# Performance work log

Hardware: AMD Instinct MI355X
Metric: run time of the kernel (lower is better)

## Reference

```python
import jax, jax.numpy as jnp
import numpy as np

N = 10000; E = 320000
DIM = 176; ATT = 16; SH_HEADS = 16; TH = 4; NH = SH_HEADS + TH; VD = DIM // SH_HEADS
LMAX = 3; NSPH = (LMAX + 1) ** 2; ZDIM = 16; RDIM = 16
RSTART = 0.8; CUT = 5.0; NLAYERS = 2


def _ln(x):
    mu = jnp.mean(x, axis=-1, keepdims=True)
    dx = x - mu
    var = jnp.mean(dx ** 2, axis=-1, keepdims=True)
    return dx * (1e-6 + var) ** (-0.5)


def _sph(v):
    # real spherical harmonics up to l=3, unnormalized overall scale, [E,16]
    x, y, z = v[..., 0], v[..., 1], v[..., 2]
    s3 = np.float32(np.sqrt(3.0)); s15 = np.float32(np.sqrt(15.0))
    c1 = np.float32(np.sqrt(5.0 / 8.0)); c2 = np.float32(np.sqrt(3.0 / 8.0))
    x2, y2, z2 = x * x, y * y, z * z
    return jnp.stack([
        jnp.ones_like(x),
        x, y, z,
        s3 * x * y, s3 * y * z, 0.5 * (3.0 * z2 - 1.0), s3 * x * z, 0.5 * s3 * (x2 - y2),
        c1 * y * (3.0 * x2 - y2), s15 * x * y * z, c2 * y * (5.0 * z2 - 1.0),
        0.5 * z * (5.0 * z2 - 3.0), c2 * x * (5.0 * z2 - 1.0),
        0.5 * s15 * z * (x2 - y2), c1 * x * (x2 - 3.0 * y2),
    ], axis=-1)


def setup_inputs() -> dict:
    key = jax.random.key(0)
    ks = jax.random.split(key, 32)

    def rn(k, shape):
        fan_in = shape[0] if len(shape) > 1 else shape[0]
        return jax.random.normal(k, shape, dtype=jnp.float32) / np.float32(np.sqrt(shape[0]))

    species = jax.random.randint(ks[0], (N,), 0, 64)
    edge_src = jax.random.randint(ks[1], (E,), 0, N)
    edge_dst = jax.random.randint(ks[2], (E,), 0, N)
    distances = RSTART + (CUT - RSTART) * jax.random.uniform(ks[3], (E,), dtype=jnp.float32)
    raw = jax.random.normal(ks[4], (E, 3), dtype=jnp.float32)
    dirn = raw / jnp.linalg.norm(raw, axis=-1, keepdims=True)
    vec = dirn * distances[:, None]
    switch = 0.5 * (jnp.cos(jnp.pi * distances / CUT) + 1.0)

    inp = {
        'species': species, 'distances': distances, 'switch': switch,
        'edge_src': edge_src, 'edge_dst': edge_dst, 'vec': vec,
        'z_table': jax.random.normal(ks[5], (64, ZDIM), dtype=jnp.float32),
        'w_species': rn(ks[6], (ZDIM, DIM)),
        'pos_w1_0': rn(ks[7], (RDIM, 2 * ATT)), 'pos_b1_0': jnp.zeros((2 * ATT,), jnp.float32),
        'pos_w2_0': rn(ks[8], (2 * ATT, ATT)), 'pos_b2_0': jnp.zeros((ATT,), jnp.float32),
        'wq_0': rn(ks[9], (DIM, NH * ATT)), 'wk_0': rn(ks[10], (DIM, NH * ATT)),
        'wv_0': rn(ks[11], (DIM, SH_HEADS * VD)),
        'upd_w_0': rn(ks[12], (2 * DIM, DIM)), 'upd_b_0': jnp.zeros((DIM,), jnp.float32),
        'pos_w1_1': rn(ks[13], (RDIM + TH * (LMAX + 1), 2 * ATT)), 'pos_b1_1': jnp.zeros((2 * ATT,), jnp.float32),
        'pos_w2_1': rn(ks[14], (2 * ATT, ATT)), 'pos_b2_1': jnp.zeros((ATT,), jnp.float32),
        'wq_1': rn(ks[15], (DIM, NH * ATT)), 'wk_1': rn(ks[16], (DIM, NH * ATT)),
        'wv_1': rn(ks[17], (DIM, SH_HEADS * VD)),
        'upd_w_1': rn(ks[18], (2 * DIM, DIM)), 'upd_b_1': jnp.zeros((DIM,), jnp.float32),
    }
    return inp


def reference(species, distances, switch, edge_src, edge_dst, vec,
              z_table, w_species,
              pos_w1_0, pos_b1_0, pos_w2_0, pos_b2_0, wq_0, wk_0, wv_0, upd_w_0, upd_b_0,
              pos_w1_1, pos_b1_1, pos_w2_1, pos_b2_1, wq_1, wk_1, wv_1, upd_w_1, upd_b_1):
    Nn = species.shape[0]
    Zi = z_table[species]                      # [N, ZDIM] species encoding
    xi = _ln(Zi @ w_species)                   # [N, DIM]

    vhat = vec / distances[:, None]
    Yij = _sph(vhat)                           # [E, NSPH]
    ls = np.repeat(np.arange(LMAX + 1), 2 * np.arange(LMAX + 1) + 1)
    parity = jnp.asarray(((-1.0) ** ls).astype(np.float32))  # [NSPH]

    centers = jnp.linspace(RSTART, CUT, RDIM, dtype=jnp.float32)
    sigma = np.float32((CUT - RSTART) / (RDIM - 1))
    radial = jnp.exp(-(((distances[:, None] - centers) / sigma) ** 2))  # [E, RDIM]

    Vi = jnp.zeros((Nn, TH, NSPH), jnp.float32)
    pos = [(pos_w1_0, pos_b1_0, pos_w2_0, pos_b2_0), (pos_w1_1, pos_b1_1, pos_w2_1, pos_b2_1)]
    att = [(wq_0, wk_0, wv_0, upd_w_0, upd_b_0), (wq_1, wk_1, wv_1, upd_w_1, upd_b_1)]
    inv_sqrt_d = np.float32(1.0 / np.sqrt(ATT))

    for layer in range(NLAYERS):
        pw1, pb1, pw2, pb2 = pos[layer]
        wq, wk, wv, uw, ub = att[layer]
        if layer == 0:
            ur = radial
        else:
            # tensor relative positional features: [E, TH, NSPH]
            xij2 = (Vi[edge_dst] + (parity * Vi)[edge_src]) * Yij[:, None, :]
            us = [xij2[:, :, l * l:(l + 1) * (l + 1)].sum(axis=-1) for l in range(LMAX + 1)]
            ur = jnp.concatenate([radial] + us, axis=-1)
        w = jax.nn.swish(ur @ pw1 + pb1) @ pw2 + pb2     # [E, ATT] positional encoding
        q = (xi @ wq).reshape(Nn, NH, ATT)
        k = (xi @ wk).reshape(Nn, NH, ATT)
        # multiplicative relative positional attention coefficients [E, NH]
        aij = jnp.einsum('ehd,ed->eh', q[edge_dst] * k[edge_src], w) * (switch[:, None] * inv_sqrt_d)
        a_s, a_t = aij[:, :SH_HEADS], aij[:, SH_HEADS:]
        v = (xi @ wv).reshape(Nn, SH_HEADS, VD)
        mi = jax.ops.segment_sum(a_s[:, :, None] * v[edge_src], edge_dst, num_segments=Nn)  # [N,SH,VD]
        Vi = Vi + jax.ops.segment_sum(
            a_t[:, :, None] * (Yij[:, None, :] + parity * Vi[edge_src]), edge_dst, num_segments=Nn)
        ui = jnp.concatenate([xi, mi.reshape(Nn, -1)], axis=-1)
        xi = _ln(xi + ui @ uw + ub)
    return xi
```

## Files before the change

kernel.cpp:

```cpp
#include <hip/hip_runtime.h>
#include <hip/hip_bf16.h>
#include <math.h>

#define N_NODES 10000
#define N_PAD   10048
#define N_EDGES 320000
#define DIM     176
#define ATT     16
#define SH_HEADS 16
#define THH     4
#define NH      20
#define VD      11
#define ZDIM    16
#define RDIM    16
#define QK_W    (NH*ATT)
#define QKV_W   816
#define UI_W    (2*DIM)
#define KQ      192
#define SIGINV  3.5714285714285716f
#define RSTEP   0.28f

typedef unsigned short ushort_t;
typedef __attribute__((ext_vector_type(8))) short bf16x8;
typedef __attribute__((ext_vector_type(4))) float f32x4;


__device__ __forceinline__ ushort_t f2bf(float f) {
    __hip_bfloat16 b = __float2bfloat16(f);
    return *(ushort_t*)&b;
}

__device__ __forceinline__ float bf2f(ushort_t u) {
    return __uint_as_float(((unsigned)u) << 16);
}

__device__ __forceinline__ void sph16(float x, float y, float z, float* Y) {
    const float s3  = 1.7320508075688772f;
    const float s15 = 3.872983346207417f;
    const float c1  = 0.7905694150420949f;
    const float c2  = 0.6123724356957945f;
    float x2 = x*x, y2 = y*y, z2 = z*z;
    Y[0]  = 1.0f;
    Y[1]  = x;
    Y[2]  = y;
    Y[3]  = z;
    Y[4]  = s3 * x * y;
    Y[5]  = s3 * y * z;
    Y[6]  = 0.5f * (3.0f * z2 - 1.0f);
    Y[7]  = s3 * x * z;
    Y[8]  = 0.5f * s3 * (x2 - y2);
    Y[9]  = c1 * y * (3.0f * x2 - y2);
    Y[10] = s15 * x * y * z;
    Y[11] = c2 * y * (5.0f * z2 - 1.0f);
    Y[12] = 0.5f * z * (5.0f * z2 - 3.0f);
    Y[13] = c2 * x * (5.0f * z2 - 1.0f);
    Y[14] = 0.5f * s15 * z * (x2 - y2);
    Y[15] = c1 * x * (x2 - 3.0f * y2);
}

__device__ __forceinline__ void unpack8(const uint4 u, float* f) {
    f[0] = __uint_as_float(u.x << 16);
    f[1] = __uint_as_float(u.x & 0xffff0000u);
    f[2] = __uint_as_float(u.y << 16);
    f[3] = __uint_as_float(u.y & 0xffff0000u);
    f[4] = __uint_as_float(u.z << 16);
    f[5] = __uint_as_float(u.z & 0xffff0000u);
    f[6] = __uint_as_float(u.w << 16);
    f[7] = __uint_as_float(u.w & 0xffff0000u);
}


__global__ __launch_bounds__(256) void k_deg(const int* edst, int* deg) {
    int e = blockIdx.x * 256 + threadIdx.x;
    if (e < N_EDGES) atomicAdd(&deg[edst[e]], 1);
}

__global__ __launch_bounds__(1024) void k_scan1(const int* deg, int* incl, int* bsum) {
    __shared__ int sd[1024];
    int b = blockIdx.x, tid = threadIdx.x;
    int gi = b * 1024 + tid;
    int v = (gi < N_NODES) ? deg[gi] : 0;
    sd[tid] = v;
    __syncthreads();
    for (int s = 1; s < 1024; s <<= 1) {
        int add = (tid >= s) ? sd[tid - s] : 0;
        __syncthreads();
        sd[tid] += add;
        __syncthreads();
    }
    if (gi < N_NODES) incl[gi] = sd[tid];
    if (tid == 1023) bsum[b] = sd[1023];
}

__global__ __launch_bounds__(1024) void k_scan3(const int* deg, const int* incl, const int* bsum,
                                                int* off, int* cursor) {
    __shared__ int bpre_s;
    int b = blockIdx.x, tid = threadIdx.x;
    if (tid == 0) {
        int acc = 0;
        for (int k = 0; k < b; k++) acc += bsum[k];
        bpre_s = acc;
    }
    __syncthreads();
    int gi = b * 1024 + tid;
    if (gi < N_NODES) {
        int e = bpre_s + incl[gi];
        off[gi + 1] = e;
        cursor[gi]  = e - deg[gi];
    }
    if (gi == 0) off[0] = 0;
}

__global__ __launch_bounds__(256) void k_scatter(const int* edst, int* cursor, int* elist) {
    int e = blockIdx.x * 256 + threadIdx.x;
    if (e < N_EDGES) {
        int p = atomicAdd(&cursor[edst[e]], 1);
        elist[p] = e;
    }
}

__global__ __launch_bounds__(256) void k_reorder(const int* elist, const int* esrc, const int* edst,
        const float* dist, const float* swit, const float* vec,
        int* src_c, int* dst_c, float* dist_c, float* sc_c, float* Yf) {
    int i = blockIdx.x * 256 + threadIdx.x;
    if (i >= N_EDGES) return;
    int e = elist[i];
    float d = dist[e];
    float inv = 1.0f / d;
    float vx = vec[(size_t)e*3 + 0] * inv;
    float vy = vec[(size_t)e*3 + 1] * inv;
    float vz = vec[(size_t)e*3 + 2] * inv;
    src_c[i]  = esrc[e];
    dst_c[i]  = edst[e];
    dist_c[i] = d;
    sc_c[i]   = swit[e] * 0.25f;
    float Y[16];
    sph16(vx, vy, vz, Y);
    #pragma unroll
    for (int m = 0; m < 16; m += 4)
        *(float4*)&Yf[(size_t)i * 16 + m] = make_float4(Y[m], Y[m+1], Y[m+2], Y[m+3]);
}


__device__ __forceinline__ void prep_qkv_body(int bid, int tid, const float* wq,
        const float* wk, const float* wv, ushort_t* Wtq) {
    int id = bid * 256 + tid;
    if (id >= 192 * 832) return;
    int k = id / 832, n = id - (id / 832) * 832;
    float v = 0.0f;
    if (k < DIM && n < QKV_W)
        v = (n < 320) ? wq[k * 320 + n] : (n < 640) ? wk[k * 320 + (n - 320)]
                                                    : wv[k * DIM + (n - 640)];
    Wtq[(size_t)n * KQ + k] = f2bf(v);
}

__device__ __forceinline__ void prep_upd_body(int bid, int tid, const float* uw, ushort_t* Wtu) {
    int id = bid * 256 + tid;
    if (id >= 352 * 192) return;
    int k = id / 192, n = id - (id / 192) * 192;
    float v = (n < DIM) ? uw[k * DIM + n] : 0.0f;
    Wtu[(size_t)n * UI_W + k] = f2bf(v);
}

__device__ __forceinline__ void prep_mlp_body(int bid, int tid, const float* pw1,
        const float* pw2, ushort_t* w1T, ushort_t* w2T, int K1) {
    int id = bid * 256 + tid;
    if (id < 1024) {
        int n = id >> 5, k = id & 31;
        w1T[n * 32 + k] = (k < K1) ? f2bf(pw1[k * 32 + n]) : 0;
    } else if (id < 1536) {
        int id2 = id - 1024;
        int n = id2 >> 5, k = id2 & 31;
        w2T[n * 32 + k] = f2bf(pw2[k * 16 + n]);
    }
}

__global__ __launch_bounds__(256) void k_prep_all(
        const float* wq0, const float* wk0, const float* wv0, ushort_t* Wtq0,
        const float* wq1, const float* wk1, const float* wv1, ushort_t* Wtq1,
        const float* uw0, ushort_t* Wtu0, const float* uw1, ushort_t* Wtu1,
        const float* pw1_0, const float* pw2_0, ushort_t* w1T0, ushort_t* w2T0,
        const float* pw1_1, const float* pw2_1, ushort_t* w1T1, ushort_t* w2T1) {
    int bid = blockIdx.x, tid = threadIdx.x;
    if (bid < 624)        prep_qkv_body(bid,        tid, wq0, wk0, wv0, Wtq0);
    else if (bid < 1248)  prep_qkv_body(bid - 624,  tid, wq1, wk1, wv1, Wtq1);
    else if (bid < 1512)  prep_upd_body(bid - 1248, tid, uw0, Wtu0);
    else if (bid < 1776)  prep_upd_body(bid - 1512, tid, uw1, Wtu1);
    else if (bid < 1782)  prep_mlp_body(bid - 1776, tid, pw1_0, pw2_0, w1T0, w2T0, 16);
    else if (bid < 1788)  prep_mlp_body(bid - 1782, tid, pw1_1, pw2_1, w1T1, w2T1, 32);
}


template<int KCHUNKS, int OMODE>
__global__ __launch_bounds__(256) void k_gemm(const ushort_t* __restrict__ A, int sA,
                                              const ushort_t* __restrict__ Bt, int sB,
                                              void* __restrict__ Cv, int sC, int M, int N,
                                              ushort_t* __restrict__ qh,
                                              ushort_t* __restrict__ kh,
                                              ushort_t* __restrict__ vh) {
    __shared__ ushort_t As[64 * 40];
    __shared__ ushort_t Bs[64 * 40];
    int tid  = threadIdx.x;
    int m0   = blockIdx.y * 64, n0 = blockIdx.x * 64;
    int w    = tid >> 6, lane = tid & 63, quad = lane >> 4, c16 = lane & 15;
    int arow = tid >> 2, aseg = tid & 3;
    f32x4 acc[4] = {};
    for (int kc = 0; kc < KCHUNKS; kc++) {
        int k0 = kc * 32;
        *(uint4*)&As[arow * 40 + aseg * 8] =
            *(const uint4*)&A[(size_t)(m0 + arow) * sA + k0 + aseg * 8];
        *(uint4*)&Bs[arow * 40 + aseg * 8] =
            *(const uint4*)&Bt[(size_t)(n0 + arow) * sB + k0 + aseg * 8];
        __syncthreads();
        bf16x8 a = *(const bf16x8*)&As[(w * 16 + c16) * 40 + quad * 8];
        #pragma unroll
        for (int t = 0; t < 4; t++) {
            bf16x8 b = *(const bf16x8*)&Bs[(t * 16 + c16) * 40 + quad * 8];
            acc[t] = __builtin_amdgcn_mfma_f32_16x16x32_bf16(a, b, acc[t], 0, 0, 0);
        }
        __syncthreads();
    }
    #pragma unroll
    for (int t = 0; t < 4; t++) {
        #pragma unroll
        for (int r = 0; r < 4; r++) {
            int row = m0 + w * 16 + quad * 4 + r;
            int col = n0 + t * 16 + c16;
            if (row < M && col < N) {
                if (OMODE == 1) {
                    ushort_t bv = f2bf(acc[t][r]);
                    if (col < 320)      qh[(size_t)row * QK_W + col] = bv;
                    else if (col < 640) kh[(size_t)row * QK_W + (col - 320)] = bv;
                    else                vh[(size_t)row * DIM  + (col - 640)] = bv;
                } else {
                    ((float*)Cv)[(size_t)row * sC + col] = acc[t][r];
                }
            }
        }
    }
}


__global__ __launch_bounds__(256) void k_node_init(const int* species, const float* z_table,
                                                   const float* wsp, float* xi,
                                                   ushort_t* xib, ushort_t* cxm) {
    __shared__ float zs[16 * ZDIM];
    __shared__ float yt[16 * DIM];
    __shared__ float red[256];
    __shared__ float mus[16], rstds[16];
    int base = blockIdx.x * 16;
    int tid  = threadIdx.x;
    { int n = tid >> 4, kk = tid & 15;
      zs[tid] = z_table[species[base + n] * ZDIM + kk]; }
    __syncthreads();
    int c = tid;
    if (c < DIM) {
        float acc[16];
        #pragma unroll
        for (int n = 0; n < 16; n++) acc[n] = 0.0f;
        for (int kk = 0; kk < ZDIM; kk++) {
            float w = wsp[kk * DIM + c];
            #pragma unroll
            for (int n = 0; n < 16; n++) acc[n] += zs[n * ZDIM + kk] * w;
        }
        #pragma unroll
        for (int n = 0; n < 16; n++) yt[n * DIM + c] = acc[n];
    }
    __syncthreads();
    { int n2 = tid >> 4, j = tid & 15;
      float s = 0.0f;
      for (int c2 = j; c2 < DIM; c2 += 16) s += yt[n2 * DIM + c2];
      red[tid] = s; }
    __syncthreads();
    if (tid < 16) { float s = 0; for (int j = 0; j < 16; j++) s += red[tid * 16 + j]; mus[tid] = s / (float)DIM; }
    __syncthreads();
    { int n2 = tid >> 4, j = tid & 15;
      float mu = mus[n2], s = 0.0f;
      for (int c2 = j; c2 < DIM; c2 += 16) { float d = yt[n2 * DIM + c2] - mu; s += d * d; }
      red[tid] = s; }
    __syncthreads();
    if (tid < 16) { float s = 0; for (int j = 0; j < 16; j++) s += red[tid * 16 + j]; rstds[tid] = rsqrtf(s / (float)DIM + 1e-6f); }
    __syncthreads();
    if (c < DIM) {
        #pragma unroll
        for (int n = 0; n < 16; n++) {
            float val = (yt[n * DIM + c] - mus[n]) * rstds[n];
            xi[(size_t)(base + n) * DIM + c] = val;
            ushort_t bv = f2bf(val);
            xib[(size_t)(base + n) * KQ + c]   = bv;
            cxm[(size_t)(base + n) * UI_W + c] = bv;
        }
    } else if (c < KQ) {
        #pragma unroll
        for (int n = 0; n < 16; n++) xib[(size_t)(base + n) * KQ + c] = 0;
    }
}


template<bool L0>
__global__ __launch_bounds__(256) void k_edge(const float* dist_c, const float* sc_c,
        const int* src_c, const int* dst_c, const float* Yf, const ushort_t* Vih,
        const ushort_t* qh, const ushort_t* kh,
        const ushort_t* w1T, const float* pb1, const ushort_t* w2T, const float* pb2,
        ushort_t* aijh) {
    __shared__ ushort_t urS[64 * 40];
    __shared__ ushort_t Ht[4][16 * 40];
    __shared__ float    wdS[64 * 17];
    __shared__ ushort_t aS[NH][64];
    int tid  = threadIdx.x;
    int w    = tid >> 6, lane = tid & 63, quad = lane >> 4, c16 = lane & 15;
    int eb   = blockIdx.x * 64;

    if (!L0) {
        if (tid < 64) {
            int i = eb + tid;
            float d = dist_c[i];
            ushort_t u[32];
            #pragma unroll
            for (int r = 0; r < 16; r++) {
                float cc = 0.8f + (float)r * RSTEP;
                float uu = (d - cc) * SIGINV;
                u[r] = f2bf(__expf(-uu * uu));
            }
            float Y[16];
            #pragma unroll
            for (int m = 0; m < 16; m += 4) {
                float4 y = *(const float4*)&Yf[(size_t)i * 16 + m];
                Y[m] = y.x; Y[m+1] = y.y; Y[m+2] = y.z; Y[m+3] = y.w;
            }
            int s = src_c[i], t_ = dst_c[i];
            const uint4* vd4 = (const uint4*)(Vih + (size_t)t_ * 64);
            const uint4* vs4 = (const uint4*)(Vih + (size_t)s  * 64);
            #pragma unroll
            for (int th = 0; th < THH; th++) {
                float fd[16], fs[16];
                unpack8(vd4[2*th],   fd);     unpack8(vd4[2*th+1], fd+8);
                unpack8(vs4[2*th],   fs);     unpack8(vs4[2*th+1], fs+8);
                float us0 = (fd[0] + fs[0]) * Y[0];
                float us1 = 0.0f, us2 = 0.0f, us3 = 0.0f;
                #pragma unroll
                for (int m = 1; m < 4; m++)  us1 += (fd[m] - fs[m]) * Y[m];
                #pragma unroll
                for (int m = 4; m < 9; m++)  us2 += (fd[m] + fs[m]) * Y[m];
                #pragma unroll
                for (int m = 9; m < 16; m++) us3 += (fd[m] - fs[m]) * Y[m];
                u[16 + 0 * 4 + th] = f2bf(us0);
                u[16 + 1 * 4 + th] = f2bf(us1);
                u[16 + 2 * 4 + th] = f2bf(us2);
                u[16 + 3 * 4 + th] = f2bf(us3);
            }
            #pragma unroll
            for (int p = 0; p < 4; p++)
                *(uint4*)&urS[tid * 40 + p * 8] = *(uint4*)&u[p * 8];
        }
        __syncthreads();
    }

    {
        int e0 = eb + w * 16;
        bf16x8 a1;
        if (L0) {
            float d = dist_c[e0 + c16];
            #pragma unroll
            for (int j = 0; j < 8; j++) {
                int r = quad * 8 + j;
                float v = 0.0f;
                if (r < 16) { float cc = 0.8f + (float)r * RSTEP; float uu = (d - cc) * SIGINV; v = __expf(-uu * uu); }
                a1[j] = (short)f2bf(v);
            }
        } else {
            a1 = *(const bf16x8*)&urS[(w * 16 + c16) * 40 + quad * 8];
        }
        bf16x8 b0 = *(const bf16x8*)&w1T[c16 * 32 + quad * 8];
        bf16x8 b1 = *(const bf16x8*)&w1T[(16 + c16) * 32 + quad * 8];
        f32x4 acc0 = {}, acc1 = {};
        acc0 = __builtin_amdgcn_mfma_f32_16x16x32_bf16(a1, b0, acc0, 0, 0, 0);
        acc1 = __builtin_amdgcn_mfma_f32_16x16x32_bf16(a1, b1, acc1, 0, 0, 0);
        float bb0 = pb1[c16], bb1 = pb1[c16 + 16];
        #pragma unroll
        for (int r = 0; r < 4; r++) {
            int er = quad * 4 + r;
            float h0 = acc0[r] + bb0; h0 = h0 / (1.0f + __expf(-h0));
            float h1 = acc1[r] + bb1; h1 = h1 / (1.0f + __expf(-h1));
            Ht[w][er * 40 + c16]      = f2bf(h0);
            Ht[w][er * 40 + 16 + c16] = f2bf(h1);
        }
        __syncthreads();
        bf16x8 a2 = *(const bf16x8*)&Ht[w][c16 * 40 + quad * 8];
        bf16x8 b2 = *(const bf16x8*)&w2T[c16 * 32 + quad * 8];
        f32x4 acc2 = {};
        acc2 = __builtin_amdgcn_mfma_f32_16x16x32_bf16(a2, b2, acc2, 0, 0, 0);
        float bb2 = pb2[c16];
        #pragma unroll
        for (int r = 0; r < 4; r++) {
            int er = quad * 4 + r;
            wdS[(w * 16 + er) * 17 + c16] = (acc2[r] + bb2) * sc_c[e0 + er];
        }
    }
    __syncthreads();

    {
        int le = tid >> 2, part = tid & 3;
        int i  = eb + le;
        int s = src_c[i], t_ = dst_c[i];
        float wd[16];
        #pragma unroll
        for (int p = 0; p < 16; p++) wd[p] = wdS[le * 17 + p];
        const uint4* q4 = (const uint4*)(qh + (size_t)t_ * QK_W);
        const uint4* k4 = (const uint4*)(kh + (size_t)s  * QK_W);
        #pragma unroll
        for (int j = 0; j < 5; j++) {
            int h = part * 5 + j;
            float qa[8], qb[8], ka[8], kb[8];
            unpack8(q4[2*h],   qa); unpack8(q4[2*h+1], qb);
            unpack8(k4[2*h],   ka); unpack8(k4[2*h+1], kb);
            float acc = 0.0f;
            #pragma unroll
            for (int dd = 0; dd < 8; dd++) acc += qa[dd] * ka[dd] * wd[dd];
            #pragma unroll
            for (int dd = 0; dd < 8; dd++) acc += qb[dd] * kb[dd] * wd[8 + dd];
            aS[h][le] = f2bf(acc);
        }
    }
    __syncthreads();
    {
        const uint* aSw = (const uint*)aS;
        for (int idx = tid; idx < NH * 32; idx += 256) {
            int h = idx >> 5, w2 = idx & 31;
            *(uint*)(aijh + (size_t)h * N_EDGES + eb + w2 * 2) = aSw[h * 32 + w2];
        }
    }
}


__device__ __forceinline__ void mi_step(int i, int c0, bool f1, bool f2,
        const int* src_c, const ushort_t* aA, const ushort_t* aB, const ushort_t* vh,
        float& acc0, float& acc1, float& acc2, float& acc3) {
    int s0 = src_c[i];
    uint2 v0 = *(const uint2*)(vh + (size_t)s0 * DIM + c0);
    float a00 = bf2f(aA[i]), a0B = bf2f(aB[i]);
    float g01 = f1 ? a0B : a00, g02 = f2 ? a0B : a00;
    acc0 += a00 * __uint_as_float(v0.x << 16);
    acc1 += g01 * __uint_as_float(v0.x & 0xffff0000u);
    acc2 += g02 * __uint_as_float(v0.y << 16);
    acc3 += a0B * __uint_as_float(v0.y & 0xffff0000u);
}

__device__ __forceinline__ void mi_wave(int n, int lane, const int* off, const int* src_c,
        const ushort_t* aijh, const ushort_t* vh, ushort_t* cxm) {
    if (lane >= 44) return;
    int c0 = lane * 4;
    int hA = c0 / VD;
    int hB = (c0 + 3) / VD;
    bool f1 = ((c0 + 1) / VD) != hA;
    bool f2 = ((c0 + 2) / VD) != hA;
    const ushort_t* aA = aijh + (size_t)hA * N_EDGES;
    const ushort_t* aB = aijh + (size_t)hB * N_EDGES;
    int start = off[n], end = off[n + 1];
    float acc0 = 0, acc1 = 0, acc2 = 0, acc3 = 0;
    int i = start;
    for (; i + 4 <= end; i += 4) {
        int s0 = src_c[i], s1 = src_c[i+1], s2 = src_c[i+2], s3 = src_c[i+3];
        uint2 v0 = *(const uint2*)(vh + (size_t)s0 * DIM + c0);
        uint2 v1 = *(const uint2*)(vh + (size_t)s1 * DIM + c0);
        uint2 v2 = *(const uint2*)(vh + (size_t)s2 * DIM + c0);
        uint2 v3 = *(const uint2*)(vh + (size_t)s3 * DIM + c0);
        float aA0 = bf2f(aA[i]),   aB0 = bf2f(aB[i]);
        float aA1 = bf2f(aA[i+1]), aB1 = bf2f(aB[i+1]);
        float aA2 = bf2f(aA[i+2]), aB2 = bf2f(aB[i+2]);
        float aA3 = bf2f(aA[i+3]), aB3 = bf2f(aB[i+3]);
        float g01 = f1 ? aB0 : aA0, g02 = f2 ? aB0 : aA0;
        float g11 = f1 ? aB1 : aA1, g12 = f2 ? aB1 : aA1;
        float g21 = f1 ? aB2 : aA2, g22 = f2 ? aB2 : aA2;
        float g31 = f1 ? aB3 : aA3, g32 = f2 ? aB3 : aA3;
        acc0 += aA0 * __uint_as_float(v0.x << 16);
        acc1 += g01 * __uint_as_float(v0.x & 0xffff0000u);
        acc2 += g02 * __uint_as_float(v0.y << 16);
        acc3 += aB0 * __uint_as_float(v0.y & 0xffff0000u);
        acc0 += aA1 * __uint_as_float(v1.x << 16);
        acc1 += g11 * __uint_as_float(v1.x & 0xffff0000u);
        acc2 += g12 * __uint_as_float(v1.y << 16);
        acc3 += aB1 * __uint_as_float(v1.y & 0xffff0000u);
        acc0 += aA2 * __uint_as_float(v2.x << 16);
        acc1 += g21 * __uint_as_float(v2.x & 0xffff0000u);
        acc2 += g22 * __uint_as_float(v2.y << 16);
        acc3 += aB2 * __uint_as_float(v2.y & 0xffff0000u);
        acc0 += aA3 * __uint_as_float(v3.x << 16);
        acc1 += g31 * __uint_as_float(v3.x & 0xffff0000u);
        acc2 += g32 * __uint_as_float(v3.y << 16);
        acc3 += aB3 * __uint_as_float(v3.y & 0xffff0000u);
    }
    for (; i < end; i++)
        mi_step(i, c0, f1, f2, src_c, aA, aB, vh, acc0, acc1, acc2, acc3);
    ushort_t o[4] = {f2bf(acc0), f2bf(acc1), f2bf(acc2), f2bf(acc3)};
    *(uint2*)(cxm + (size_t)n * UI_W + DIM + c0) = *(uint2*)o;
}

__device__ __forceinline__ void vi_wave(int n, int lane, const int* off,
        const float* Yf, const ushort_t* aijh, ushort_t* Vih) {
    int th = lane >> 4, sm = lane & 15;
    const ushort_t* ah = aijh + (size_t)(SH_HEADS + th) * N_EDGES;
    int start = off[n], end = off[n + 1];
    float acc = 0.0f;
    int i = start;
    for (; i + 4 <= end; i += 4) {
        float a0 = bf2f(ah[i]),   y0 = Yf[(size_t)i * 16 + sm];
        float a1 = bf2f(ah[i+1]), y1 = Yf[(size_t)(i+1) * 16 + sm];
        float a2 = bf2f(ah[i+2]), y2 = Yf[(size_t)(i+2) * 16 + sm];
        float a3 = bf2f(ah[i+3]), y3 = Yf[(size_t)(i+3) * 16 + sm];
        acc += a0 * y0 + a1 * y1 + a2 * y2 + a3 * y3;
    }
    for (; i < end; i++)
        acc += bf2f(ah[i]) * Yf[(size_t)i * 16 + sm];
    Vih[(size_t)n * 64 + lane] = f2bf(acc);
}

__global__ __launch_bounds__(256) void k_agg0(const int* off, const int* src_c,
        const float* Yf, const ushort_t* aijh, const ushort_t* vh,
        ushort_t* cxm, ushort_t* Vih) {
    int wid  = blockIdx.x * 4 + (threadIdx.x >> 6);
    int lane = threadIdx.x & 63;
    if (wid < N_NODES)
        mi_wave(wid, lane, off, src_c, aijh, vh, cxm);
    else
        vi_wave(wid - N_NODES, lane, off, Yf, aijh, Vih);
}

__global__ __launch_bounds__(256) void k_agg1(const int* off, const int* src_c,
        const ushort_t* aijh, const ushort_t* vh, ushort_t* cxm) {
    int wid  = blockIdx.x * 4 + (threadIdx.x >> 6);
    int lane = threadIdx.x & 63;
    mi_wave(wid, lane, off, src_c, aijh, vh, cxm);
}


__global__ __launch_bounds__(256) void k_lnfinal(const float* yg, const float* xi,
        const float* ub, float* xo, ushort_t* xib, ushort_t* cxm) {
    __shared__ float yt[16 * DIM];
    __shared__ float red[256];
    __shared__ float mus[16], rstds[16];
    int base = blockIdx.x * 16;
    int tid  = threadIdx.x;
    for (int idx = tid; idx < 16 * DIM; idx += 256) {
        int n = idx / DIM, c = idx - n * DIM;
        yt[idx] = xi[(size_t)(base + n) * DIM + c]
                + yg[(size_t)(base + n) * DIM + c] + ub[c];
    }
    __syncthreads();
    { int n2 = tid >> 4, j = tid & 15;
      float s = 0.0f;
      for (int c2 = j; c2 < DIM; c2 += 16) s += yt[n2 * DIM + c2];
      red[tid] = s; }
    __syncthreads();
    if (tid < 16) { float s = 0; for (int j = 0; j < 16; j++) s += red[tid * 16 + j]; mus[tid] = s / (float)DIM; }
    __syncthreads();
    { int n2 = tid >> 4, j = tid & 15;
      float mu = mus[n2], s = 0.0f;
      for (int c2 = j; c2 < DIM; c2 += 16) { float d = yt[n2 * DIM + c2] - mu; s += d * d; }
      red[tid] = s; }
    __syncthreads();
    if (tid < 16) { float s = 0; for (int j = 0; j < 16; j++) s += red[tid * 16 + j]; rstds[tid] = rsqrtf(s / (float)DIM + 1e-6f); }
    __syncthreads();
    int c = tid;
    if (c < DIM) {
        #pragma unroll
        for (int n = 0; n < 16; n++) {
            float val = (yt[n * DIM + c] - mus[n]) * rstds[n];
            xo[(size_t)(base + n) * DIM + c] = val;
            ushort_t bv = f2bf(val);
            xib[(size_t)(base + n) * KQ + c]   = bv;
            cxm[(size_t)(base + n) * UI_W + c] = bv;
        }
    } else if (c < KQ) {
        #pragma unroll
        for (int n = 0; n < 16; n++) xib[(size_t)(base + n) * KQ + c] = 0;
    }
}


extern "C" void kernel_launch(void* const* d_in, const int* in_sizes, int n_in,
                              void* d_out, int out_size, void* d_ws, size_t ws_size,
                              hipStream_t stream) {
    const int*   species = (const int*)  d_in[0];
    const float* dist    = (const float*)d_in[1];
    const float* swit    = (const float*)d_in[2];
    const int*   esrc    = (const int*)  d_in[3];
    const int*   edst    = (const int*)  d_in[4];
    const float* vec     = (const float*)d_in[5];
    const float* z_table = (const float*)d_in[6];
    const float* wsp     = (const float*)d_in[7];
    const float* pw1_0 = (const float*)d_in[8],  *pb1_0 = (const float*)d_in[9];
    const float* pw2_0 = (const float*)d_in[10], *pb2_0 = (const float*)d_in[11];
    const float* wq0 = (const float*)d_in[12], *wk0 = (const float*)d_in[13];
    const float* wv0 = (const float*)d_in[14], *uw0 = (const float*)d_in[15];
    const float* ub0 = (const float*)d_in[16];
    const float* pw1_1 = (const float*)d_in[17], *pb1_1 = (const float*)d_in[18];
    const float* pw2_1 = (const float*)d_in[19], *pb2_1 = (const float*)d_in[20];
    const float* wq1 = (const float*)d_in[21], *wk1 = (const float*)d_in[22];
    const float* wv1 = (const float*)d_in[23], *uw1 = (const float*)d_in[24];
    const float* ub1 = (const float*)d_in[25];
    float* out = (float*)d_out;

    char* p = (char*)d_ws;
    auto alloc = [&](size_t bytes) -> char* {
        char* r = p;
        p += (bytes + 255) & ~(size_t)255;
        return r;
    };
    int* deg    = (int*)alloc((size_t)N_NODES * 4);
    int* incl   = (int*)alloc((size_t)N_NODES * 4);
    int* bsum   = (int*)alloc(64);
    int* off    = (int*)alloc((size_t)(N_NODES + 1) * 4);
    int* cursor = (int*)alloc((size_t)N_NODES * 4);
    int* elist  = (int*)alloc((size_t)N_EDGES * 4);
    int*   src_c  = (int*)  alloc((size_t)N_EDGES * 4);
    int*   dst_c  = (int*)  alloc((size_t)N_EDGES * 4);
    float* dist_c = (float*)alloc((size_t)N_EDGES * 4);
    float* sc_c   = (float*)alloc((size_t)N_EDGES * 4);
    float* Yf     = (float*)alloc((size_t)N_EDGES * 16 * 4);
    float* xiA  = (float*)alloc((size_t)N_NODES * DIM * 4);
    float* xiB  = (float*)alloc((size_t)N_NODES * DIM * 4);
    ushort_t* xib  = (ushort_t*)alloc((size_t)N_PAD * KQ * 2);
    ushort_t* cxm  = (ushort_t*)alloc((size_t)N_PAD * UI_W * 2);
    ushort_t* qh   = (ushort_t*)alloc((size_t)N_NODES * QK_W * 2);
    ushort_t* kh   = (ushort_t*)alloc((size_t)N_NODES * QK_W * 2);
    ushort_t* vh   = (ushort_t*)alloc((size_t)N_NODES * DIM * 2);
    float* ybuf    = (float*)alloc((size_t)N_NODES * DIM * 4);
    ushort_t* Wtq0 = (ushort_t*)alloc((size_t)832 * KQ * 2);
    ushort_t* Wtq1 = (ushort_t*)alloc((size_t)832 * KQ * 2);
    ushort_t* Wtu0 = (ushort_t*)alloc((size_t)192 * UI_W * 2);
    ushort_t* Wtu1 = (ushort_t*)alloc((size_t)192 * UI_W * 2);
    ushort_t* w1T0 = (ushort_t*)alloc((size_t)32 * 32 * 2);
    ushort_t* w2T0 = (ushort_t*)alloc((size_t)16 * 32 * 2);
    ushort_t* w1T1 = (ushort_t*)alloc((size_t)32 * 32 * 2);
    ushort_t* w2T1 = (ushort_t*)alloc((size_t)16 * 32 * 2);
    ushort_t* Vih  = (ushort_t*)alloc((size_t)N_NODES * 64 * 2);
    ushort_t* aijh = (ushort_t*)alloc((size_t)N_EDGES * NH * 2);

    const int NB_E  = (N_EDGES + 255) / 256;
    const int NB_F  = N_EDGES / 64;
    const int NB_T  = N_NODES / 16;
    const dim3 GRID_QKV(13, 157);
    const dim3 GRID_UPD(3, 157);

    hipMemsetAsync(deg, 0, (size_t)N_NODES * 4, stream);
    k_deg<<<NB_E, 256, 0, stream>>>(edst, deg);
    k_scan1<<<10, 1024, 0, stream>>>(deg, incl, bsum);
    k_scan3<<<10, 1024, 0, stream>>>(deg, incl, bsum, off, cursor);
    k_scatter<<<NB_E, 256, 0, stream>>>(edst, cursor, elist);
    k_reorder<<<NB_E, 256, 0, stream>>>(elist, esrc, edst, dist, swit, vec,
                                        src_c, dst_c, dist_c, sc_c, Yf);

    k_prep_all<<<1788, 256, 0, stream>>>(wq0, wk0, wv0, Wtq0, wq1, wk1, wv1, Wtq1,
                                         uw0, Wtu0, uw1, Wtu1,
                                         pw1_0, pw2_0, w1T0, w2T0,
                                         pw1_1, pw2_1, w1T1, w2T1);

    k_node_init<<<NB_T, 256, 0, stream>>>(species, z_table, wsp, xiA, xib, cxm);

    k_gemm<6, 1><<<GRID_QKV, 256, 0, stream>>>(xib, KQ, Wtq0, KQ, nullptr, 0,
                                               N_NODES, QKV_W, qh, kh, vh);
    k_edge<true><<<NB_F, 256, 0, stream>>>(dist_c, sc_c, src_c, dst_c, Yf, Vih,
                                           qh, kh, w1T0, pb1_0, w2T0, pb2_0, aijh);
    k_agg0<<<5000, 256, 0, stream>>>(off, src_c, Yf, aijh, vh, cxm, Vih);
    k_gemm<11, 0><<<GRID_UPD, 256, 0, stream>>>(cxm, UI_W, Wtu0, UI_W, ybuf, DIM,
                                                N_NODES, DIM, nullptr, nullptr, nullptr);
    k_lnfinal<<<NB_T, 256, 0, stream>>>(ybuf, xiA, ub0, xiB, xib, cxm);

    k_gemm<6, 1><<<GRID_QKV, 256, 0, stream>>>(xib, KQ, Wtq1, KQ, nullptr, 0,
                                               N_NODES, QKV_W, qh, kh, vh);
    k_edge<false><<<NB_F, 256, 0, stream>>>(dist_c, sc_c, src_c, dst_c, Yf, Vih,
                                            qh, kh, w1T1, pb1_1, w2T1, pb2_1, aijh);
    k_agg1<<<2500, 256, 0, stream>>>(off, src_c, aijh, vh, cxm);
    k_gemm<11, 0><<<GRID_UPD, 256, 0, stream>>>(cxm, UI_W, Wtu1, UI_W, ybuf, DIM,
                                                N_NODES, DIM, nullptr, nullptr, nullptr);
    k_lnfinal<<<NB_T, 256, 0, stream>>>(ybuf, xiB, ub1, out, xib, cxm);
}
```

Baseline: 422.4 us.

## Store q/k in fp16 and use packed dot2 for edge attention scores

The projection GEMM now writes q and k as fp16 instead of bf16, and the edge kernel computes q*k*w with packed half multiplies plus fdot2 accumulation rather than unpacking to fp32. The positional weights are stored in shared memory as fp16, with padded strides for the weight and score buffers to avoid bank conflicts. The layer>0 tensor-feature stage is spread across all 256 threads (one tensor head per wave) instead of only 64. This trims ALU and unpack work and idle threads in the edge kernel, at the cost of fp16 range and precision in the q*k product.

Result: no change. 430.4 us (+1.9%).

```diff
diff --git a/kernel.cpp b/kernel.cpp
--- a/kernel.cpp
+++ b/kernel.cpp
@@ -23,6 +23,7 @@
 typedef unsigned short ushort_t;
 typedef __attribute__((ext_vector_type(8))) short bf16x8;
 typedef __attribute__((ext_vector_type(4))) float f32x4;
+typedef __attribute__((ext_vector_type(2))) _Float16 half2v;
 
 
 __device__ __forceinline__ ushort_t f2bf(float f) {
@@ -32,6 +33,21 @@
 
 __device__ __forceinline__ float bf2f(ushort_t u) {
     return __uint_as_float(((unsigned)u) << 16);
+}
+
+__device__ __forceinline__ ushort_t f2h(float f) {
+    _Float16 h = (_Float16)f;
+    return *(ushort_t*)&h;
+}
+
+__device__ __forceinline__ float dot2acc(uint a, uint b, uint w, float acc) {
+    half2v pa = *(half2v*)&a, pb = *(half2v*)&b, pw = *(half2v*)&w;
+    half2v pr = pa * pb;
+#if __has_builtin(__builtin_amdgcn_fdot2)
+    return __builtin_amdgcn_fdot2(pr, pw, acc, false);
+#else
+    return acc + (float)pr.x * (float)pw.x + (float)pr.y * (float)pw.y;
+#endif
 }
 
 __device__ __forceinline__ void sph16(float x, float y, float z, float* Y) {
@@ -228,10 +244,9 @@
             int col = n0 + t * 16 + c16;
             if (row < M && col < N) {
                 if (OMODE == 1) {
-                    ushort_t bv = f2bf(acc[t][r]);
-                    if (col < 320)      qh[(size_t)row * QK_W + col] = bv;
-                    else if (col < 640) kh[(size_t)row * QK_W + (col - 320)] = bv;
-                    else                vh[(size_t)row * DIM  + (col - 640)] = bv;
+                    if (col < 320)      qh[(size_t)row * QK_W + col] = f2h(acc[t][r]);
+                    else if (col < 640) kh[(size_t)row * QK_W + (col - 320)] = f2h(acc[t][r]);
+                    else                vh[(size_t)row * DIM  + (col - 640)] = f2bf(acc[t][r]);
                 } else {
                     ((float*)Cv)[(size_t)row * sC + col] = acc[t][r];
                 }
@@ -305,54 +320,51 @@
         ushort_t* aijh) {
     __shared__ ushort_t urS[64 * 40];
     __shared__ ushort_t Ht[4][16 * 40];
-    __shared__ float    wdS[64 * 17];
-    __shared__ ushort_t aS[NH][64];
+    __shared__ uint     wdU[64 * 9];
+    __shared__ uint     aSu[NH * 33];
+    ushort_t* wdHS = (ushort_t*)wdU;
+    ushort_t* aS   = (ushort_t*)aSu;
     int tid  = threadIdx.x;
     int w    = tid >> 6, lane = tid & 63, quad = lane >> 4, c16 = lane & 15;
     int eb   = blockIdx.x * 64;
 
     if (!L0) {
-        if (tid < 64) {
-            int i = eb + tid;
-            float d = dist_c[i];
-            ushort_t u[32];
-            #pragma unroll
-            for (int r = 0; r < 16; r++) {
-                float cc = 0.8f + (float)r * RSTEP;
-                float uu = (d - cc) * SIGINV;
-                u[r] = f2bf(__expf(-uu * uu));
-            }
-            float Y[16];
-            #pragma unroll
-            for (int m = 0; m < 16; m += 4) {
-                float4 y = *(const float4*)&Yf[(size_t)i * 16 + m];
-                Y[m] = y.x; Y[m+1] = y.y; Y[m+2] = y.z; Y[m+3] = y.w;
-            }
-            int s = src_c[i], t_ = dst_c[i];
-            const uint4* vd4 = (const uint4*)(Vih + (size_t)t_ * 64);
-            const uint4* vs4 = (const uint4*)(Vih + (size_t)s  * 64);
-            #pragma unroll
-            for (int th = 0; th < THH; th++) {
-                float fd[16], fs[16];
-                unpack8(vd4[2*th],   fd);     unpack8(vd4[2*th+1], fd+8);
-                unpack8(vs4[2*th],   fs);     unpack8(vs4[2*th+1], fs+8);
-                float us0 = (fd[0] + fs[0]) * Y[0];
-                float us1 = 0.0f, us2 = 0.0f, us3 = 0.0f;
-                #pragma unroll
-                for (int m = 1; m < 4; m++)  us1 += (fd[m] - fs[m]) * Y[m];
-                #pragma unroll
-                for (int m = 4; m < 9; m++)  us2 += (fd[m] + fs[m]) * Y[m];
-                #pragma unroll
-                for (int m = 9; m < 16; m++) us3 += (fd[m] - fs[m]) * Y[m];
-                u[16 + 0 * 4 + th] = f2bf(us0);
-                u[16 + 1 * 4 + th] = f2bf(us1);
-                u[16 + 2 * 4 + th] = f2bf(us2);
-                u[16 + 3 * 4 + th] = f2bf(us3);
-            }
-            #pragma unroll
-            for (int p = 0; p < 4; p++)
-                *(uint4*)&urS[tid * 40 + p * 8] = *(uint4*)&u[p * 8];
-        }
+        int le = tid & 63, th = tid >> 6;
+        int i = eb + le;
+        float d = dist_c[i];
+        ushort_t ur4[4];
+        #pragma unroll
+        for (int rr = 0; rr < 4; rr++) {
+            int r = th * 4 + rr;
+            float cc = 0.8f + (float)r * RSTEP;
+            float uu = (d - cc) * SIGINV;
+            ur4[rr] = f2bf(__expf(-uu * uu));
+        }
+        *(uint2*)&urS[le * 40 + th * 4] = *(uint2*)ur4;
+        float Y[16];
+        #pragma unroll
+        for (int m = 0; m < 16; m += 4) {
+            float4 y = *(const float4*)&Yf[(size_t)i * 16 + m];
+            Y[m] = y.x; Y[m+1] = y.y; Y[m+2] = y.z; Y[m+3] = y.w;
+        }
+        int s = src_c[i], t_ = dst_c[i];
+        const uint4* vd4 = (const uint4*)(Vih + (size_t)t_ * 64);
+        const uint4* vs4 = (const uint4*)(Vih + (size_t)s  * 64);
+        float fd[16], fs[16];
+        unpack8(vd4[2*th],   fd); unpack8(vd4[2*th+1], fd+8);
+        unpack8(vs4[2*th],   fs); unpack8(vs4[2*th+1], fs+8);
+        float us0 = (fd[0] + fs[0]) * Y[0];
+        float us1 = 0.0f, us2 = 0.0f, us3 = 0.0f;
+        #pragma unroll
+        for (int m = 1; m < 4; m++)  us1 += (fd[m] - fs[m]) * Y[m];
+        #pragma unroll
+        for (int m = 4; m < 9; m++)  us2 += (fd[m] + fs[m]) * Y[m];
+        #pragma unroll
+        for (int m = 9; m < 16; m++) us3 += (fd[m] - fs[m]) * Y[m];
+        urS[le * 40 + 16 + 0 * 4 + th] = f2bf(us0);
+        urS[le * 40 + 16 + 1 * 4 + th] = f2bf(us1);
+        urS[le * 40 + 16 + 2 * 4 + th] = f2bf(us2);
+        urS[le * 40 + 16 + 3 * 4 + th] = f2bf(us3);
         __syncthreads();
     }
 
@@ -394,7 +406,7 @@
         #pragma unroll
         for (int r = 0; r < 4; r++) {
             int er = quad * 4 + r;
-            wdS[(w * 16 + er) * 17 + c16] = (acc2[r] + bb2) * sc_c[e0 + er];
+            wdHS[(w * 16 + er) * 18 + c16] = f2h((acc2[r] + bb2) * sc_c[e0 + er]);
         }
     }
     __syncthreads();
@@ -403,31 +415,34 @@
         int le = tid >> 2, part = tid & 3;
         int i  = eb + le;
         int s = src_c[i], t_ = dst_c[i];
-        float wd[16];
-        #pragma unroll
-        for (int p = 0; p < 16; p++) wd[p] = wdS[le * 17 + p];
+        const uint* wdp_ = wdU + le * 9;
+        uint wdp[8];
+        #pragma unroll
+        for (int p2 = 0; p2 < 8; p2++) wdp[p2] = wdp_[p2];
         const uint4* q4 = (const uint4*)(qh + (size_t)t_ * QK_W);
         const uint4* k4 = (const uint4*)(kh + (size_t)s  * QK_W);
         #pragma unroll
         for (int j = 0; j < 5; j++) {
             int h = part * 5 + j;
-            float qa[8], qb[8], ka[8], kb[8];
-            unpack8(q4[2*h],   qa); unpack8(q4[2*h+1], qb);
-            unpack8(k4[2*h],   ka); unpack8(k4[2*h+1], kb);
+            uint4 qa = q4[2*h], qb = q4[2*h+1];
+            uint4 ka = k4[2*h], kb = k4[2*h+1];
             float acc = 0.0f;
-            #pragma unroll
-            for (int dd = 0; dd < 8; dd++) acc += qa[dd] * ka[dd] * wd[dd];
-            #pragma unroll
-            for (int dd = 0; dd < 8; dd++) acc += qb[dd] * kb[dd] * wd[8 + dd];
-            aS[h][le] = f2bf(acc);
+            acc = dot2acc(qa.x, ka.x, wdp[0], acc);
+            acc = dot2acc(qa.y, ka.y, wdp[1], acc);
+            acc = dot2acc(qa.z, ka.z, wdp[2], acc);
+            acc = dot2acc(qa.w, ka.w, wdp[3], acc);
+            acc = dot2acc(qb.x, kb.x, wdp[4], acc);
+            acc = dot2acc(qb.y, kb.y, wdp[5], acc);
+            acc = dot2acc(qb.z, kb.z, wdp[6], acc);
+            acc = dot2acc(qb.w, kb.w, wdp[7], acc);
+            aS[h * 66 + le] = f2bf(acc);
         }
     }
     __syncthreads();
     {
-        const uint* aSw = (const uint*)aS;
         for (int idx = tid; idx < NH * 32; idx += 256) {
             int h = idx >> 5, w2 = idx & 31;
-            *(uint*)(aijh + (size_t)h * N_EDGES + eb + w2 * 2) = aSw[h * 32 + w2];
+            *(uint*)(aijh + (size_t)h * N_EDGES + eb + w2 * 2) = aSu[h * 33 + w2];
         }
     }
 }
```
